# Kernel optimization log

Measured on AMD Instinct MI355X. Metric: run time of the kernel, lower is better.

## Reference

```python
import jax, jax.numpy as jnp
import numpy as np

DT = 0.001          # continuous-dynamics step (dt > 0 branch)
KERNEL_SIZE = 16384 # L
P, H = 1024, 256    # d_state, d_input (= d_output)


def setup_inputs() -> dict:
    key = jax.random.key(0)
    kAr, kAi, kB, kC = jax.random.split(key, 4)
    # Continuous diagonal state matrix: real part in [strong, weak] = [-0.5, -0.01] (stable),
    # imaginary part uniform in [-pi, pi] (mimics diagonal_state_space_matrix init).
    Ar = jax.random.uniform(kAr, (P,), minval=-0.5, maxval=-0.01)
    Ai = jax.random.uniform(kAi, (P,), minval=-np.pi, maxval=np.pi)
    A = jnp.stack([Ar, Ai], axis=-1).astype(jnp.float32)            # (P, 2) view_as_real
    # B, C ~ uniform disk (radius 1): scaled complex gaussians are a fine stand-in numerically.
    B = (jax.random.normal(kB, (P, H, 2)) / np.sqrt(H)).astype(jnp.float32)   # (P, H, 2)
    C = (jax.random.normal(kC, (H, P, 2)) / np.sqrt(P)).astype(jnp.float32)   # (H, P, 2)
    return {"A": A, "B": B, "C": C}


def _as_complex(x):
    return x[..., 0] + 1j * x[..., 1]


def reference(A, B, C):
    """Vandermonde SSM kernel generation (continuous dt > 0 branch).
    Returns kernel (H, L, 2) = real view of complex kernel (H, L)."""
    Ac = _as_complex(A)   # (P,) complex
    Bc = _as_complex(B)   # (P, H)
    Cc = _as_complex(C)   # (H, P)

    # ZOH-style discretization
    A_bar = jnp.exp(Ac * DT)                               # (P,)
    B_bar = ((A_bar - 1.0) / Ac)[:, None] * Bc             # (P, H)

    # Vandermonde matrix V[p, l] = A_bar[p] ** l  (complex power == exp(l * log(a)))
    powers = jnp.arange(KERNEL_SIZE, dtype=jnp.float32)    # (L,)
    V = jnp.exp(jnp.log(A_bar)[:, None] * powers[None, :]) # (P, L)

    # W[h, p] = C[h, p] * B_bar[p, h]; kernel[h, l] = sum_p W[h, p] * V[p, l]
    W = Cc * B_bar.T                                       # (H, P)
    kernel = jnp.einsum('hp,pl->hl', W, V)                 # (H, L) complex
    return jnp.stack([kernel.real, kernel.imag], axis=-1)  # (H, L, 2) float32
```

## Files before the change

kernel.cpp:

```cpp
#include <hip/hip_runtime.h>
#include <hip/hip_fp16.h>

#define P_DIM 1024
#define H_DIM 256
#define L_DIM 16384
#define DT 0.001f
#define TWOPI 6.283185307179586f
#define INV2PI 0.15915494309189535f
#define WSCALE 4096.0f
#define INV_WSCALE (1.0f / 4096.0f)
#define BM 128
#define BN 128
#define BK 64
#define NT 256

typedef _Float16 f16x8 __attribute__((ext_vector_type(8)));
typedef float f32x4 __attribute__((ext_vector_type(4)));

#define GPTR(p) (const __attribute__((address_space(1))) unsigned*)(p)
#define LPTR(p) (__attribute__((address_space(3))) unsigned*)(p)

union H2U { __half2 h; unsigned u; };

__device__ __forceinline__ float2 cmulf(float2 a, float2 b) {
    return make_float2(a.x * b.x - a.y * b.y, a.x * b.y + a.y * b.x);
}

__global__ __launch_bounds__(256)
void prep_kernel(const float* __restrict__ Ag, const float* __restrict__ Bg,
                 const float* __restrict__ Cg, __half* __restrict__ W2) {
    __shared__ float2 Bt[64][33];
    __shared__ float2 sc[64];
    const int t  = threadIdx.x;
    const int p0 = (blockIdx.x & 15) << 6;
    const int h0 = (blockIdx.x >> 4) << 5;

    if (t < 64) {
        float2 a = ((const float2*)Ag)[p0 + t];
        float er = __expf(a.x * DT);
        float s, c; __sincosf(a.y * DT, &s, &c);
        float nr = er * c - 1.f, ni = er * s;
        float inv = 1.f / (a.x * a.x + a.y * a.y);
        sc[t] = make_float2((nr * a.x + ni * a.y) * inv, (ni * a.x - nr * a.y) * inv);
    }
    #pragma unroll
    for (int i = 0; i < 8; ++i) {
        int idx = i * 256 + t, p = idx >> 5, h = idx & 31;
        Bt[p][h] = ((const float2*)Bg)[(size_t)(p0 + p) * H_DIM + h0 + h];
    }
    __syncthreads();
    #pragma unroll
    for (int i = 0; i < 8; ++i) {
        int idx = i * 256 + t, h = idx >> 6, p = idx & 63;
        float2 cc = ((const float2*)Cg)[(size_t)(h0 + h) * P_DIM + p0 + p];
        float2 s2 = sc[p], b = Bt[p][h];
        float2 tv = cmulf(cc, s2);
        float wr = (tv.x * b.x - tv.y * b.y) * WSCALE;
        float wi = (tv.x * b.y + tv.y * b.x) * WSCALE;
        ((__half2*)W2)[(size_t)(h0 + h) * P_DIM + p0 + p] =
            __float22half2_rn(make_float2(wr, wi));
    }
}

__global__ __launch_bounds__(NT, 2)
void vand_mfma_kernel(const float* __restrict__ Ag,
                      const _Float16* __restrict__ W2,
                      float* __restrict__ out) {
    __shared__ __attribute__((aligned(16))) _Float16 As[2][BM * BK];
    __shared__ __attribute__((aligned(16))) _Float16 Bs[2][BN * BK];
    __shared__ float4 Atab[P_DIM];

    const int tid  = threadIdx.x;
    const int lane = tid & 63;
    const int w    = tid >> 6;
    const int wm   = w & 1, wn = w >> 1;
    const int m0   = blockIdx.y * BM;
    const int nb   = blockIdx.x * BN;
    const int lb   = blockIdx.x * (BN / 2);

    const float2* Ag2 = (const float2*)Ag;

    #pragma unroll
    for (int i = 0; i < 4; ++i) {
        int p = tid + i * 256;
        float2 a = Ag2[p];
        float e = __expf(a.x * DT);
        float s, c; __sincosf(a.y * DT, &s, &c);
        Atab[p] = make_float4(e * c, e * s, a.x * DT, a.y * (DT * INV2PI));
    }

    f32x4 acc[4][4];
    #pragma unroll
    for (int mt = 0; mt < 4; ++mt)
        #pragma unroll
        for (int nt = 0; nt < 4; ++nt)
            acc[mt][nt] = (f32x4){0.f, 0.f, 0.f, 0.f};

    const int pl    = tid & 31;
    const int lg    = tid >> 5;
    const float l0f = (float)(lb + lg * 8);
    const int cq3   = (pl >> 2) << 3;
    const int cs    = (2 * pl) & 7;
    const int vbase = lg * 1024 + cs;

    const int goff = (lane >> 3) * 2048 + (((lane & 7) ^ (lane >> 3)) << 3);
    const _Float16* gwbase = W2 + (size_t)(m0 + (w << 5)) * 2048;
    const int ldsoff = (w << 5) * 64;

    _Float16* Acur = &As[0][0]; _Float16* Bcur = &Bs[0][0];
    _Float16* Anxt = &As[1][0]; _Float16* Bnxt = &Bs[1][0];

#define DMA_CHUNK(K0, DST)                                                        \
    {                                                                             \
        const _Float16* gw = gwbase + (K0) + goff;                                \
        _Float16* lB = (DST) + ldsoff;                                            \
        _Pragma("unroll")                                                         \
        for (int r = 0; r < 4; ++r)                                               \
            __builtin_amdgcn_global_load_lds(GPTR(gw + r * 8 * 2048),             \
                                             LPTR(lB + r * 8 * 64), 16, 0, 0);    \
    }

#define VGEN_CHUNK(K0, DST)                                                       \
    {                                                                             \
        const int pg = ((K0) >> 1) + pl;                                          \
        float4 t4 = Atab[pg];                                                     \
        float mg = __expf(t4.z * l0f);                                            \
        float x  = t4.w * l0f; x -= rintf(x);                                     \
        float s, c; __sincosf(x * TWOPI, &s, &c);                                 \
        float2 v  = make_float2(mg * c, mg * s);                                  \
        float2 ab = make_float2(t4.x, t4.y);                                      \
        _Pragma("unroll")                                                         \
        for (int j = 0; j < 8; ++j) {                                             \
            H2U u0, u1;                                                           \
            u0.h = __float22half2_rn(make_float2(v.x, -v.y));                     \
            u1.h = __float22half2_rn(make_float2(v.y, v.x));                      \
            int e0 = vbase + j * 128 + (cq3 ^ (((2 * j) & 7) << 3));              \
            int e1 = vbase + j * 128 + 64 + (cq3 ^ (((2 * j + 1) & 7) << 3));     \
            *(unsigned*)((DST) + e0) = u0.u;                                      \
            *(unsigned*)((DST) + e1) = u1.u;                                      \
            if (j < 7) v = cmulf(v, ab);                                          \
        }                                                                         \
    }

    DMA_CHUNK(0, Acur)
    __syncthreads();
    VGEN_CHUNK(0, Bcur)

    for (int kk = 0; kk < 32; ++kk) {
        if (kk < 31) {
            const int k1 = (kk + 1) * BK;
            DMA_CHUNK(k1, Anxt)
            VGEN_CHUNK(k1, Bnxt)
            asm volatile("s_waitcnt vmcnt(4) lgkmcnt(0)" ::: "memory");
        } else {
            asm volatile("s_waitcnt vmcnt(0) lgkmcnt(0)" ::: "memory");
        }
        __builtin_amdgcn_sched_barrier(0);
        __builtin_amdgcn_s_barrier();
        __builtin_amdgcn_sched_barrier(0);

        __builtin_amdgcn_s_setprio(1);
        #pragma unroll
        for (int ks = 0; ks < 2; ++ks) {
            f16x8 af[4], bf[4];
            const int g = ks * 4 + (lane >> 4);
            #pragma unroll
            for (int t = 0; t < 4; ++t) {
                int m = wm * 64 + t * 16 + (lane & 15);
                af[t] = *(const f16x8*)(Acur + m * 64 + ((g ^ (m & 7)) << 3));
                int n = wn * 64 + t * 16 + (lane & 15);
                bf[t] = *(const f16x8*)(Bcur + n * 64 + ((g ^ (n & 7)) << 3));
            }
            #pragma unroll
            for (int mt = 0; mt < 4; ++mt)
                #pragma unroll
                for (int nt = 0; nt < 4; ++nt)
                    acc[mt][nt] = __builtin_amdgcn_mfma_f32_16x16x32_f16(
                        af[mt], bf[nt], acc[mt][nt], 0, 0, 0);
        }
        __builtin_amdgcn_s_setprio(0);
        __builtin_amdgcn_sched_barrier(0);
        __builtin_amdgcn_s_barrier();
        __builtin_amdgcn_sched_barrier(0);

        _Float16* tA = Acur; Acur = Anxt; Anxt = tA;
        _Float16* tB = Bcur; Bcur = Bnxt; Bnxt = tB;
    }

    #pragma unroll
    for (int mt = 0; mt < 4; ++mt) {
        #pragma unroll
        for (int nt = 0; nt < 4; ++nt) {
            int h = m0 + wm * 64 + mt * 16 + ((lane >> 4) << 2);
            int n = nb + wn * 64 + nt * 16 + (lane & 15);
            #pragma unroll
            for (int r = 0; r < 4; ++r)
                out[(size_t)(h + r) * 32768 + n] = acc[mt][nt][r] * INV_WSCALE;
        }
    }
#undef DMA_CHUNK
#undef VGEN_CHUNK
}

extern "C" void kernel_launch(void* const* d_in, const int* in_sizes, int n_in,
                              void* d_out, int out_size, void* d_ws, size_t ws_size,
                              hipStream_t stream) {
    const float* A = (const float*)d_in[0];
    const float* B = (const float*)d_in[1];
    const float* C = (const float*)d_in[2];
    float* out = (float*)d_out;
    __half* W2 = (__half*)d_ws;

    prep_kernel<<<dim3(128), dim3(256), 0, stream>>>(A, B, C, W2);
    vand_mfma_kernel<<<dim3(L_DIM * 2 / BN, H_DIM / BM), dim3(NT), 0, stream>>>(
        A, (const _Float16*)W2, out);
}
```

Before: 107.9 us.

## Interleave Vandermonde generation between the two MFMA halves of each K step

The generation of the next Vandermonde tile (exp/sincos plus a complex-multiply chain written to LDS) moves from before the barrier to between the two MFMA sub-steps of the current tile. This lets its VALU/transcendental work overlap with matrix-core execution instead of running serially before it. Wait counts are reorganised so LDS writes are drained before the end-of-iteration barrier, and an extra barrier is added after the prologue. Setprio now brackets only the MFMA loops. The risk is that the compiler serialises the two halves anyway, or that register pressure rises from interleaving.

```diff
diff --git a/kernel.cpp b/kernel.cpp
--- a/kernel.cpp
+++ b/kernel.cpp
@@ -142,43 +142,53 @@
         }                                                                         \
     }
 
+#define MFMA_HALF(KS)                                                             \
+    {                                                                             \
+        f16x8 af[4], bf[4];                                                       \
+        const int g = (KS) * 4 + (lane >> 4);                                     \
+        _Pragma("unroll")                                                         \
+        for (int t = 0; t < 4; ++t) {                                             \
+            int m = wm * 64 + t * 16 + (lane & 15);                               \
+            af[t] = *(const f16x8*)(Acur + m * 64 + ((g ^ (m & 7)) << 3));        \
+            int n = wn * 64 + t * 16 + (lane & 15);                               \
+            bf[t] = *(const f16x8*)(Bcur + n * 64 + ((g ^ (n & 7)) << 3));        \
+        }                                                                         \
+        __builtin_amdgcn_s_setprio(1);                                            \
+        _Pragma("unroll")                                                         \
+        for (int mt = 0; mt < 4; ++mt)                                            \
+            _Pragma("unroll")                                                     \
+            for (int nt = 0; nt < 4; ++nt)                                        \
+                acc[mt][nt] = __builtin_amdgcn_mfma_f32_16x16x32_f16(             \
+                    af[mt], bf[nt], acc[mt][nt], 0, 0, 0);                        \
+        __builtin_amdgcn_s_setprio(0);                                            \
+    }
+
     DMA_CHUNK(0, Acur)
     __syncthreads();
     VGEN_CHUNK(0, Bcur)
+    asm volatile("s_waitcnt lgkmcnt(0)" ::: "memory");
+    __builtin_amdgcn_sched_barrier(0);
+    __builtin_amdgcn_s_barrier();
+    __builtin_amdgcn_sched_barrier(0);
 
     for (int kk = 0; kk < 32; ++kk) {
         if (kk < 31) {
-            const int k1 = (kk + 1) * BK;
-            DMA_CHUNK(k1, Anxt)
-            VGEN_CHUNK(k1, Bnxt)
-            asm volatile("s_waitcnt vmcnt(4) lgkmcnt(0)" ::: "memory");
+            DMA_CHUNK((kk + 1) * BK, Anxt)
+            asm volatile("s_waitcnt vmcnt(4)" ::: "memory");
         } else {
-            asm volatile("s_waitcnt vmcnt(0) lgkmcnt(0)" ::: "memory");
+            asm volatile("s_waitcnt vmcnt(0)" ::: "memory");
         }
         __builtin_amdgcn_sched_barrier(0);
         __builtin_amdgcn_s_barrier();
         __builtin_amdgcn_sched_barrier(0);
 
-        __builtin_amdgcn_s_setprio(1);
-        #pragma unroll
-        for (int ks = 0; ks < 2; ++ks) {
-            f16x8 af[4], bf[4];
-            const int g = ks * 4 + (lane >> 4);
-            #pragma unroll
-            for (int t = 0; t < 4; ++t) {
-                int m = wm * 64 + t * 16 + (lane & 15);
-                af[t] = *(const f16x8*)(Acur + m * 64 + ((g ^ (m & 7)) << 3));
-                int n = wn * 64 + t * 16 + (lane & 15);
-                bf[t] = *(const f16x8*)(Bcur + n * 64 + ((g ^ (n & 7)) << 3));
-            }
-            #pragma unroll
-            for (int mt = 0; mt < 4; ++mt)
-                #pragma unroll
-                for (int nt = 0; nt < 4; ++nt)
-                    acc[mt][nt] = __builtin_amdgcn_mfma_f32_16x16x32_f16(
-                        af[mt], bf[nt], acc[mt][nt], 0, 0, 0);
+        MFMA_HALF(0)
+        if (kk < 31) {
+            VGEN_CHUNK((kk + 1) * BK, Bnxt)
         }
-        __builtin_amdgcn_s_setprio(0);
+        MFMA_HALF(1)
+
+        asm volatile("s_waitcnt lgkmcnt(0)" ::: "memory");
         __builtin_amdgcn_sched_barrier(0);
         __builtin_amdgcn_s_barrier();
         __builtin_amdgcn_sched_barrier(0);
@@ -200,6 +210,7 @@
     }
 #undef DMA_CHUNK
 #undef VGEN_CHUNK
+#undef MFMA_HALF
 }
 
 extern "C" void kernel_launch(void* const* d_in, const int* in_sizes, int n_in,
```

Measured after the change: 110.8 us. 2.7% more time.
